# Performance work log

Hardware: AMD Instinct MI355X
Metric: run time of the kernel (lower is better)

## Reference

```python
import jax, jax.numpy as jnp
import numpy as np

B, S, E, H = 2, 2048, 1024, 16
D = E // H  # head_dim = 64


def setup_inputs() -> dict:
    key = jax.random.key(0)
    ks = jax.random.split(key, 12)
    s = 1.0 / np.sqrt(E)
    return {
        "queries": jax.random.normal(ks[0], (B, S, E), jnp.float32),
        "keys": jax.random.normal(ks[1], (B, S, E), jnp.float32),
        "values": jax.random.normal(ks[2], (B, S, E), jnp.float32),
        "mask": jnp.zeros((B, 1, S, S), jnp.float32),
        "Wq": jax.random.normal(ks[3], (E, E), jnp.float32) * s,
        "bq": jnp.zeros((E,), jnp.float32),
        "Wk": jax.random.normal(ks[4], (E, E), jnp.float32) * s,
        "bk": jnp.zeros((E,), jnp.float32),
        "Wv": jax.random.normal(ks[5], (E, E), jnp.float32) * s,
        "bv": jnp.zeros((E,), jnp.float32),
        "Wo": jax.random.normal(ks[6], (E, E), jnp.float32) * s,
        "bo": jnp.zeros((E,), jnp.float32),
    }


def reference(queries, keys, values, mask, Wq, bq, Wk, bk, Wv, bv, Wo, bo):
    # QKV projections, then split heads: [B,S,E] -> [B,H,S,D]
    def split_heads(x):
        return x.reshape(B, S, H, D).transpose(0, 2, 1, 3)

    Q = split_heads(queries @ Wq + bq)
    K = split_heads(keys @ Wk + bk)
    V = split_heads(values @ Wv + bv)
    scale = jnp.sqrt(jnp.asarray(D, jnp.float32))
    # [B,H,S,S] attention scores
    scores = jnp.einsum("bhqd,bhkd->bhqk", Q, K) / scale
    scores = scores + mask * -10000.0
    weights = jax.nn.softmax(scores, axis=-1)
    # [B,H,S,D] -> [B,S,E]
    out = jnp.einsum("bhqk,bhkd->bhqd", weights, V)
    out = out.transpose(0, 2, 1, 3).reshape(B, S, E)
    return out @ Wo + bo
```

## Files before the change

### kernel.cpp

```cpp
#include <hip/hip_runtime.h>
#include <hip/hip_bf16.h>
#include <stdint.h>

#define B_ 2
#define S_ 2048
#define E_ 1024
#define H_ 16
#define D_ 64
#define LOG2E 1.4426950408889634f

typedef unsigned short ubf;
typedef __attribute__((ext_vector_type(8))) short bh8;
typedef __attribute__((ext_vector_type(4))) float fx4;
typedef __attribute__((ext_vector_type(16))) float fx16;

__device__ __forceinline__ ubf f2bf(float f) {
  unsigned u = __float_as_uint(f);
  unsigned r = (u + 0x7fffu + ((u >> 16) & 1u)) >> 16;
  return (ubf)r;
}

__device__ __forceinline__ unsigned cvtpk(float lo, float hi2) {
  unsigned r;
  asm("v_cvt_pk_bf16_f32 %0, %1, %2" : "=v"(r) : "v"(lo), "v"(hi2));
  return r;
}

__device__ __forceinline__ void pl32swap(unsigned& a, unsigned& b) {
  asm("v_permlane32_swap_b32 %0, %1" : "+v"(a), "+v"(b));
}

__device__ __forceinline__ void gl_lds16(const void* g, void* l) {
  __builtin_amdgcn_global_load_lds(
      (const __attribute__((address_space(1))) void*)g,
      (__attribute__((address_space(3))) void*)l, 16, 0, 0);
}

__global__ void prep(const float* __restrict__ q, const float* __restrict__ k,
                     const float* __restrict__ v, const float* __restrict__ mask,
                     ubf* __restrict__ dst0, int* __restrict__ flagarr) {
  const int z = blockIdx.z;
  const int tid = threadIdx.x;
  const int stride = gridDim.x * blockDim.x;
  if (z == 3) {
    int any = 0;
    const int n4m = (B_ * S_ * S_) / 4;
    for (int j = blockIdx.x * blockDim.x + tid; j < n4m; j += stride) {
      float4 x = ((const float4*)mask)[j];
      any |= (x.x != 0.f) | (x.y != 0.f) | (x.z != 0.f) | (x.w != 0.f);
    }
    int wany = __any(any != 0) ? 1 : 0;
    if ((tid & 63) == 0) flagarr[blockIdx.x * 4 + (tid >> 6)] = wany;
    return;
  }
  const float* src = (z == 0) ? q : (z == 1) ? k : v;
  ubf* dst = dst0 + (size_t)z * (B_ * S_ * E_);
  const int n4 = (B_ * S_ * E_) / 4;
  for (int j = blockIdx.x * blockDim.x + tid; j < n4; j += stride) {
    float4 x = ((const float4*)src)[j];
    ushort4 o;
    o.x = f2bf(x.x); o.y = f2bf(x.y); o.z = f2bf(x.z); o.w = f2bf(x.w);
    ((ushort4*)dst)[j] = o;
  }
}

__global__ void wtrans4(const float* __restrict__ Wq, const float* __restrict__ Wk,
                        const float* __restrict__ Wv, const float* __restrict__ Wo,
                        ubf* __restrict__ Wt0) {
  __shared__ float t[32][33];
  int z = blockIdx.z;
  const float* W = (z == 0) ? Wq : (z == 1) ? Wk : (z == 2) ? Wv : Wo;
  ubf* Wt = Wt0 + (size_t)z * (E_ * E_);
  int kb = blockIdx.x, nb = blockIdx.y;
  int c = threadIdx.x & 31, r0 = threadIdx.x >> 5;
#pragma unroll
  for (int rr = 0; rr < 32; rr += 8)
    t[r0 + rr][c] = W[(size_t)(kb * 32 + r0 + rr) * E_ + nb * 32 + c];
  __syncthreads();
#pragma unroll
  for (int rr = 0; rr < 32; rr += 8)
    Wt[(size_t)(nb * 32 + r0 + rr) * E_ + kb * 32 + c] = f2bf(t[c][r0 + rr]);
}

__global__ void __launch_bounds__(256)
gemm_qkv(const ubf* __restrict__ X, const ubf* __restrict__ Wt,
         const float* __restrict__ bq, const float* __restrict__ bk,
         const float* __restrict__ bv, ubf* __restrict__ Out) {
  constexpr int K = 1024;
  __shared__ ubf Asm[2][128 * 32];
  __shared__ ubf Bsm[2][128 * 32];
  const int z = blockIdx.z;
  const ubf* A  = (z == 2) ? (Wt + 2u * 1048576u) : (X + (size_t)z * 4194304u);
  const ubf* Bt = (z == 2) ? (X + 2u * 4194304u) : (Wt + (size_t)z * 1048576u);
  const float* bias = (z == 0) ? bq : (z == 1) ? bk : bv;
  ubf* Cout = Out + (size_t)z * 4194304u;
  const int bm = (z == 2) ? blockIdx.y : blockIdx.x;
  const int bn = (z == 2) ? blockIdx.x : blockIdx.y;

  const int tid = threadIdx.x;
  const int lane = tid & 63, w = tid >> 6;
  const int wm = w >> 1, wn = w & 1;
  const int g = lane >> 4, c15 = lane & 15;

  const fx4 FZ = {0.f, 0.f, 0.f, 0.f};
  fx4 acc[4][4];
#pragma unroll
  for (int m = 0; m < 4; m++)
#pragma unroll
    for (int n = 0; n < 4; n++) acc[m][n] = FZ;

  auto stage = [&](int buf, int k0) {
#pragma unroll
    for (int i = 0; i < 2; i++) {
      int s = i * 256 + tid;
      int row = s >> 2, cc = s & 3;
      int sc = cc ^ (row & 3);
      gl_lds16(A + (size_t)(bm * 128 + row) * K + k0 + sc * 8,
               (char*)&Asm[buf][0] + (i * 256 + (tid & 192)) * 16);
      gl_lds16(Bt + (size_t)(bn * 128 + row) * K + k0 + sc * 8,
               (char*)&Bsm[buf][0] + (i * 256 + (tid & 192)) * 16);
    }
  };

  stage(0, 0);
  __syncthreads();
  for (int t = 0; t < K / 32; t++) {
    int cur = t & 1;
    if (t + 1 < K / 32) stage(cur ^ 1, (t + 1) * 32);
    bh8 a[4], b[4];
#pragma unroll
    for (int m = 0; m < 4; m++) {
      int row = wm * 64 + m * 16 + c15;
      int ch = g ^ (row & 3);
      a[m] = *(const bh8*)((const char*)&Asm[cur][0] + row * 64 + ch * 16);
    }
#pragma unroll
    for (int n = 0; n < 4; n++) {
      int row = wn * 64 + n * 16 + c15;
      int ch = g ^ (row & 3);
      b[n] = *(const bh8*)((const char*)&Bsm[cur][0] + row * 64 + ch * 16);
    }
#pragma unroll
    for (int m = 0; m < 4; m++)
#pragma unroll
      for (int n = 0; n < 4; n++)
        acc[m][n] = __builtin_amdgcn_mfma_f32_16x16x32_bf16(a[m], b[n], acc[m][n], 0, 0, 0);
    __syncthreads();
  }

#pragma unroll
  for (int m = 0; m < 4; m++) {
    int rbase = bm * 128 + wm * 64 + m * 16 + g * 4;
#pragma unroll
    for (int n = 0; n < 4; n++) {
      int col = bn * 128 + wn * 64 + n * 16 + c15;
#pragma unroll
      for (int r = 0; r < 4; r++) {
        int mrow = rbase + r;
        float val = acc[m][n][r];
        if (z <= 1) {
          val = val + bias[col];
          if (z == 0) val *= 0.125f * LOG2E;
          int bb = mrow >> 11, ss = mrow & 2047, hh = col >> 6, dd = col & 63;
          Cout[((size_t)(bb * H_ + hh) * S_ + ss) * D_ + dd] = f2bf(val);
        } else {
          val = val + bias[mrow];
          int bb = col >> 11, ss = col & 2047, hh = mrow >> 6, dd = mrow & 63;
          Cout[((size_t)(bb * H_ + hh) * D_ + dd) * S_ + ss] = f2bf(val);
        }
      }
    }
  }
}

__global__ void __launch_bounds__(256)
gemm_out(const ubf* __restrict__ A, const ubf* __restrict__ Bt,
         const float* __restrict__ bias, float* __restrict__ Cout, int N) {
  constexpr int K = 1024;
  __shared__ ubf Asm[2][128 * 32];
  __shared__ ubf Bsm[2][128 * 32];
  const int tid = threadIdx.x;
  const int lane = tid & 63, w = tid >> 6;
  const int wm = w >> 1, wn = w & 1;
  const int bm = blockIdx.y, bn = blockIdx.x;
  const int g = lane >> 4, c15 = lane & 15;

  const fx4 FZ = {0.f, 0.f, 0.f, 0.f};
  fx4 acc[4][4];
#pragma unroll
  for (int m = 0; m < 4; m++)
#pragma unroll
    for (int n = 0; n < 4; n++) acc[m][n] = FZ;

  auto stage = [&](int buf, int k0) {
#pragma unroll
    for (int i = 0; i < 2; i++) {
      int s = i * 256 + tid;
      int row = s >> 2, cc = s & 3;
      int sc = cc ^ (row & 3);
      gl_lds16(A + (size_t)(bm * 128 + row) * K + k0 + sc * 8,
               (char*)&Asm[buf][0] + (i * 256 + (tid & 192)) * 16);
      gl_lds16(Bt + (size_t)(bn * 128 + row) * K + k0 + sc * 8,
               (char*)&Bsm[buf][0] + (i * 256 + (tid & 192)) * 16);
    }
  };

  stage(0, 0);
  __syncthreads();
  for (int t = 0; t < K / 32; t++) {
    int cur = t & 1;
    if (t + 1 < K / 32) stage(cur ^ 1, (t + 1) * 32);
    bh8 a[4], b[4];
#pragma unroll
    for (int m = 0; m < 4; m++) {
      int row = wm * 64 + m * 16 + c15;
      int ch = g ^ (row & 3);
      a[m] = *(const bh8*)((const char*)&Asm[cur][0] + row * 64 + ch * 16);
    }
#pragma unroll
    for (int n = 0; n < 4; n++) {
      int row = wn * 64 + n * 16 + c15;
      int ch = g ^ (row & 3);
      b[n] = *(const bh8*)((const char*)&Bsm[cur][0] + row * 64 + ch * 16);
    }
#pragma unroll
    for (int m = 0; m < 4; m++)
#pragma unroll
      for (int n = 0; n < 4; n++)
        acc[m][n] = __builtin_amdgcn_mfma_f32_16x16x32_bf16(a[m], b[n], acc[m][n], 0, 0, 0);
    __syncthreads();
  }

#pragma unroll
  for (int m = 0; m < 4; m++) {
    int rbase = bm * 128 + wm * 64 + m * 16 + g * 4;
#pragma unroll
    for (int n = 0; n < 4; n++) {
      int col = bn * 128 + wn * 64 + n * 16 + c15;
#pragma unroll
      for (int r = 0; r < 4; r++)
        Cout[(size_t)(rbase + r) * N + col] = acc[m][n][r] + bias[col];
    }
  }
}

#define ROWQ(r) (((r) & 3) + 8 * ((r) >> 2) + 4 * hi)

#define PV_STEP(KF, W0, W1, W2, W3)                                             \
    {                                                                           \
      unsigned wa[4] = {W0, W1, W2, W3};                                        \
      bh8 pa = *(bh8*)wa;                                                       \
      int ch = (2 * (KF) + hi) ^ (l31 & 7);                                     \
      bh8 bv0 = *(const bh8*)(Vc + l31 * 128 + ch * 16);                        \
      acc0 = __builtin_amdgcn_mfma_f32_32x32x16_bf16(pa, bv0, acc0, 0, 0, 0);   \
      bh8 bv1 = *(const bh8*)(Vc + (32 + l31) * 128 + ch * 16);                 \
      acc1 = __builtin_amdgcn_mfma_f32_32x32x16_bf16(pa, bv1, acc1, 0, 0, 0);   \
    }

__global__ void __launch_bounds__(256, 4)
flash_fast(const ubf* __restrict__ Q, const ubf* __restrict__ Kh,
           const ubf* __restrict__ Vt, float* __restrict__ O0,
           float* __restrict__ O1, float2* __restrict__ ml) {
  __shared__ ubf Ksm[2][64 * 64];
  __shared__ ubf Vsm[2][64 * 64];
  const int tid = threadIdx.x, lane = tid & 63, w = tid >> 6;
  const int l31 = lane & 31, hi = lane >> 5;
  const int bh = blockIdx.x;
  const int qb = blockIdx.y;
  const int half = blockIdx.z;
  const int qg = qb * 128 + w * 32 + l31;
  const int k00 = half * (S_ / 2);
  constexpr int NT = (S_ / 2) / 64;

  const ubf* Qrow = Q + ((size_t)bh * S_ + qg) * D_;
  bh8 q4[4];
#pragma unroll
  for (int kf = 0; kf < 4; kf++) q4[kf] = *(const bh8*)(Qrow + kf * 16 + hi * 8);

  fx16 acc0, acc1, ZF;
#pragma unroll
  for (int i = 0; i < 16; i++) { acc0[i] = 0.f; acc1[i] = 0.f; ZF[i] = 0.f; }
  float2 lr2 = make_float2(0.f, 0.f);

  const ubf* Kg = Kh + (size_t)bh * S_ * D_;
  const ubf* Vg = Vt + (size_t)bh * D_ * S_;

  auto stage = [&](int buf, int k0) {
#pragma unroll
    for (int i = 0; i < 2; i++) {
      int s = i * 256 + tid;
      int row = s >> 3, cc = s & 7;
      int sw = cc ^ (row & 7);
      gl_lds16(Kg + (size_t)(k0 + row) * D_ + sw * 8,
               (char*)&Ksm[buf][0] + (i * 256 + (tid & 192)) * 16);
      gl_lds16(Vg + (size_t)row * S_ + k0 + sw * 8,
               (char*)&Vsm[buf][0] + (i * 256 + (tid & 192)) * 16);
    }
  };

  stage(0, k00);

  for (int t = 0; t < NT; t++) {
    int cur = t & 1;
    if (t + 1 < NT) {
      stage(cur ^ 1, k00 + (t + 1) * 64);
      asm volatile("s_waitcnt vmcnt(4)" ::: "memory");
    } else {
      asm volatile("s_waitcnt vmcnt(0)" ::: "memory");
    }
    __builtin_amdgcn_s_barrier();
    const char* Kc = (const char*)&Ksm[cur][0];
    const char* Vc = (const char*)&Vsm[cur][0];

#pragma unroll
    for (int h2 = 0; h2 < 2; h2++) {
      fx16 sc;
      __builtin_amdgcn_s_setprio(1);
      {
        int ch = hi ^ (l31 & 7);
        bh8 ak = *(const bh8*)(Kc + (h2 * 32 + l31) * 128 + ch * 16);
        sc = __builtin_amdgcn_mfma_f32_32x32x16_bf16(ak, q4[0], ZF, 0, 0, 0);
      }
#pragma unroll
      for (int kf = 1; kf < 4; kf++) {
        int ch = (2 * kf + hi) ^ (l31 & 7);
        bh8 ak = *(const bh8*)(Kc + (h2 * 32 + l31) * 128 + ch * 16);
        sc = __builtin_amdgcn_mfma_f32_32x32x16_bf16(ak, q4[kf], sc, 0, 0, 0);
      }
      __builtin_amdgcn_s_setprio(0);

#pragma unroll
      for (int i = 0; i < 8; i++) {
        float p0 = exp2f(sc[2 * i]);
        float p1 = exp2f(sc[2 * i + 1]);
        sc[2 * i] = p0; sc[2 * i + 1] = p1;
        lr2.x += p0; lr2.y += p1;
      }

      unsigned pk[8];
#pragma unroll
      for (int i = 0; i < 8; i++) pk[i] = cvtpk(sc[2 * i], sc[2 * i + 1]);
      pl32swap(pk[0], pk[2]); pl32swap(pk[1], pk[3]);
      pl32swap(pk[4], pk[6]); pl32swap(pk[5], pk[7]);

      __builtin_amdgcn_s_setprio(1);
      PV_STEP(2 * h2,     pk[0], pk[1], pk[2], pk[3])
      PV_STEP(2 * h2 + 1, pk[4], pk[5], pk[6], pk[7])
      __builtin_amdgcn_s_setprio(0);
    }
    __builtin_amdgcn_s_barrier();
  }

  float lrun = lr2.x + lr2.y;
  float lsum = lrun + __shfl_xor(lrun, 32);
  float* Obase = half ? O1 : O0;
#pragma unroll
  for (int r = 0; r < 16; r++) {
    int q2 = ROWQ(r);
    size_t rowbase = ((size_t)bh * S_ + qb * 128 + w * 32 + q2) * D_;
    Obase[rowbase + l31] = acc0[r];
    Obase[rowbase + 32 + l31] = acc1[r];
  }
  if (hi == 0) {
    int sq = qb * 128 + w * 32 + l31;
    ml[(size_t)half * (32 * S_) + bh * S_ + sq] = make_float2(0.0f, lsum);
  }
}

__global__ void __launch_bounds__(256)
combine(const float* __restrict__ O0, const float* __restrict__ O1,
        const float2* __restrict__ ml, ubf* __restrict__ AO) {
  int tid = blockIdx.x * 256 + threadIdx.x;
  int row = tid >> 4, dq = tid & 15;
  int bh = row >> 11, s = row & 2047;
  float2 m0 = ml[row];
  float2 m1 = ml[32 * S_ + row];
  float m = fmaxf(m0.x, m1.x);
  float w0 = exp2f(m0.x - m), w1 = exp2f(m1.x - m);
  float inv = 1.0f / (m0.y * w0 + m1.y * w1);
  float4 a = *(const float4*)(O0 + (size_t)row * D_ + dq * 4);
  float4 c = *(const float4*)(O1 + (size_t)row * D_ + dq * 4);
  ushort4 o;
  o.x = f2bf((a.x * w0 + c.x * w1) * inv);
  o.y = f2bf((a.y * w0 + c.y * w1) * inv);
  o.z = f2bf((a.z * w0 + c.z * w1) * inv);
  o.w = f2bf((a.w * w0 + c.w * w1) * inv);
  int b_ = bh >> 4, h = bh & 15;
  *(ushort4*)(AO + ((size_t)(b_ * S_ + s)) * E_ + h * 64 + dq * 4) = o;
}

__global__ void __launch_bounds__(256, 4)
flash_masked(const ubf* __restrict__ Q, const ubf* __restrict__ Kh,
             const ubf* __restrict__ Vt, const float* __restrict__ mask,
             const int* __restrict__ flagarr, ubf* __restrict__ AO) {
  __shared__ int anyf;
  if (threadIdx.x == 0) anyf = 0;
  __syncthreads();
  {
    int a = 0;
#pragma unroll
    for (int i = 0; i < 8; i++) a |= flagarr[threadIdx.x + i * 256];
    if (a) anyf = 1;
  }
  __syncthreads();
  if (anyf == 0) return;

  __shared__ ubf Ksm[2][64 * 64];
  __shared__ ubf Vsm[2][64 * 64];
  const int tid = threadIdx.x, lane = tid & 63, w = tid >> 6;
  const int l31 = lane & 31, hi = lane >> 5;
  const int bh = blockIdx.x;
  const int qb = blockIdx.y;
  const int b = bh >> 4, h = bh & 15;
  const int qg = qb * 128 + w * 32 + l31;
  constexpr int NT = S_ / 64;

  const ubf* Qrow = Q + ((size_t)bh * S_ + qg) * D_;
  bh8 q4[4];
#pragma unroll
  for (int kf = 0; kf < 4; kf++) q4[kf] = *(const bh8*)(Qrow + kf * 16 + hi * 8);

  fx16 acc0, acc1;
#pragma unroll
  for (int i = 0; i < 16; i++) { acc0[i] = 0.f; acc1[i] = 0.f; }
  float mrun = -3.0e38f, lrun = 0.f;

  const ubf* Kg = Kh + (size_t)bh * S_ * D_;
  const ubf* Vg = Vt + (size_t)bh * D_ * S_;

  auto stage = [&](int buf, int k0) {
#pragma unroll
    for (int i = 0; i < 2; i++) {
      int s = i * 256 + tid;
      int row = s >> 3, cc = s & 7;
      int sw = cc ^ (row & 7);
      gl_lds16(Kg + (size_t)(k0 + row) * D_ + sw * 8,
               (char*)&Ksm[buf][0] + (i * 256 + (tid & 192)) * 16);
      gl_lds16(Vg + (size_t)row * S_ + k0 + sw * 8,
               (char*)&Vsm[buf][0] + (i * 256 + (tid & 192)) * 16);
    }
  };

  stage(0, 0);
  __syncthreads();

  for (int t = 0; t < NT; t++) {
    int cur = t & 1;
    if (t + 1 < NT) stage(cur ^ 1, (t + 1) * 64);
    const char* Kc = (const char*)&Ksm[cur][0];
    const char* Vc = (const char*)&Vsm[cur][0];

#pragma unroll
    for (int h2 = 0; h2 < 2; h2++) {
      fx16 sc;
#pragma unroll
      for (int i = 0; i < 16; i++) sc[i] = 0.f;
#pragma unroll
      for (int kf = 0; kf < 4; kf++) {
        int ch = (2 * kf + hi) ^ (l31 & 7);
        bh8 ak = *(const bh8*)(Kc + (h2 * 32 + l31) * 128 + ch * 16);
        sc = __builtin_amdgcn_mfma_f32_32x32x16_bf16(ak, q4[kf], sc, 0, 0, 0);
      }
      const float* mq = mask + ((size_t)(b * S_ + qg)) * S_ + t * 64 + h2 * 32;
#pragma unroll
      for (int r = 0; r < 16; r++)
        sc[r] += mq[ROWQ(r)] * (-14426.950408889634f);

      float pm = sc[0];
#pragma unroll
      for (int r = 1; r < 16; r++) pm = fmaxf(pm, sc[r]);
      pm = fmaxf(pm, __shfl_xor(pm, 32));
      if (__any(pm - mrun > 11.5415603f)) {
        float mnew = fmaxf(mrun, pm);
        float al = exp2f(mrun - mnew);
        lrun *= al;
#pragma unroll
        for (int r = 0; r < 16; r++) {
          float alr = __shfl(al, ROWQ(r));
          acc0[r] *= alr;
          acc1[r] *= alr;
        }
        mrun = mnew;
      }
      float rsv[4] = {0.f, 0.f, 0.f, 0.f};
#pragma unroll
      for (int i = 0; i < 16; i++) {
        float p = exp2f(sc[i] - mrun);
        sc[i] = p;
        rsv[i & 3] += p;
      }
      lrun += (rsv[0] + rsv[1]) + (rsv[2] + rsv[3]);

      unsigned pk[8];
#pragma unroll
      for (int i = 0; i < 8; i++) pk[i] = cvtpk(sc[2 * i], sc[2 * i + 1]);
      pl32swap(pk[0], pk[2]); pl32swap(pk[1], pk[3]);
      pl32swap(pk[4], pk[6]); pl32swap(pk[5], pk[7]);

      PV_STEP(2 * h2,     pk[0], pk[1], pk[2], pk[3])
      PV_STEP(2 * h2 + 1, pk[4], pk[5], pk[6], pk[7])
    }
    __syncthreads();
  }

  float ltot = lrun + __shfl_xor(lrun, 32);
#pragma unroll
  for (int r = 0; r < 16; r++) {
    int q2 = ROWQ(r);
    float linv = 1.0f / __shfl(ltot, q2);
    size_t base = ((size_t)(b * S_ + qb * 128 + w * 32 + q2)) * E_ + h * 64;
    AO[base + l31] = f2bf(acc0[r] * linv);
    AO[base + 32 + l31] = f2bf(acc1[r] * linv);
  }
}

extern "C" void kernel_launch(void* const* d_in, const int* in_sizes, int n_in,
                              void* d_out, int out_size, void* d_ws, size_t ws_size,
                              hipStream_t stream) {
  (void)in_sizes; (void)n_in; (void)out_size; (void)ws_size;
  const float* q  = (const float*)d_in[0];
  const float* k  = (const float*)d_in[1];
  const float* v  = (const float*)d_in[2];
  const float* mask = (const float*)d_in[3];
  const float* Wq = (const float*)d_in[4];
  const float* bq = (const float*)d_in[5];
  const float* Wk = (const float*)d_in[6];
  const float* bk = (const float*)d_in[7];
  const float* Wv = (const float*)d_in[8];
  const float* bv = (const float*)d_in[9];
  const float* Wo = (const float*)d_in[10];
  const float* bo = (const float*)d_in[11];

  char* ws = (char*)d_ws;
  ubf* X    = (ubf*)(ws);
  ubf* Wt0  = (ubf*)(ws + 25165824);
  ubf* Qh   = (ubf*)(ws + 33554432);
  ubf* Kh   = (ubf*)(ws + 41943040);
  ubf* Vt   = (ubf*)(ws + 50331648);
  ubf* AO   = (ubf*)(ws + 58720256);
  int* flagarr = (int*)(ws + 67108864);
  float*  O0p = (float*)(ws);
  float2* mlp = (float2*)(ws + 16777216);
  float*  O1p = (float*)d_out;

  ubf* Wot = Wt0 + 3145728;

  prep<<<dim3(512, 1, 4), 256, 0, stream>>>(q, k, v, mask, X, flagarr);
  wtrans4<<<dim3(32, 32, 4), 256, 0, stream>>>(Wq, Wk, Wv, Wo, Wt0);

  gemm_qkv<<<dim3(32, 8, 3), 256, 0, stream>>>(X, Wt0, bq, bk, bv, Qh);

  flash_fast<<<dim3(32, 16, 2), 256, 0, stream>>>(Qh, Kh, Vt, O0p, O1p, mlp);
  combine<<<4096, 256, 0, stream>>>(O0p, O1p, mlp, AO);
  flash_masked<<<dim3(32, 16), 256, 0, stream>>>(Qh, Kh, Vt, mask, flagarr, AO);

  gemm_out<<<dim3(8, 32), 256, 0, stream>>>(AO, Wot, bo, (float*)d_out, 1024);
}
```

Measured before the change: 164.6 us.

## Double per-wave query rows in flash kernel and pipeline GEMM LDS staging

In flash_fast each wave now handles 64 query rows as two 32-row tiles that share every K and V fragment read from LDS. The block shrinks to 128 threads, so each thread issues four async loads per buffer, with the wait count adjusted to match. This halves LDS reads per MFMA but doubles the accumulator registers and halves the waves per block. The two GEMM kernels change their LDS swizzle to XOR on (row>>1)&3, replace __syncthreads with explicit vmcnt waits and raw barriers for prefetch overlap, and raise wave priority around the MFMA block.

```diff
diff --git a/kernel.cpp b/kernel.cpp
--- a/kernel.cpp
+++ b/kernel.cpp
@@ -114,7 +114,7 @@
     for (int i = 0; i < 2; i++) {
       int s = i * 256 + tid;
       int row = s >> 2, cc = s & 3;
-      int sc = cc ^ (row & 3);
+      int sc = cc ^ ((row >> 1) & 3);
       gl_lds16(A + (size_t)(bm * 128 + row) * K + k0 + sc * 8,
                (char*)&Asm[buf][0] + (i * 256 + (tid & 192)) * 16);
       gl_lds16(Bt + (size_t)(bn * 128 + row) * K + k0 + sc * 8,
@@ -123,29 +123,36 @@
   };
 
   stage(0, 0);
-  __syncthreads();
   for (int t = 0; t < K / 32; t++) {
     int cur = t & 1;
-    if (t + 1 < K / 32) stage(cur ^ 1, (t + 1) * 32);
+    if (t + 1 < K / 32) {
+      stage(cur ^ 1, (t + 1) * 32);
+      asm volatile("s_waitcnt vmcnt(4)" ::: "memory");
+    } else {
+      asm volatile("s_waitcnt vmcnt(0)" ::: "memory");
+    }
+    __builtin_amdgcn_s_barrier();
     bh8 a[4], b[4];
 #pragma unroll
     for (int m = 0; m < 4; m++) {
       int row = wm * 64 + m * 16 + c15;
-      int ch = g ^ (row & 3);
+      int ch = g ^ ((row >> 1) & 3);
       a[m] = *(const bh8*)((const char*)&Asm[cur][0] + row * 64 + ch * 16);
     }
 #pragma unroll
     for (int n = 0; n < 4; n++) {
       int row = wn * 64 + n * 16 + c15;
-      int ch = g ^ (row & 3);
+      int ch = g ^ ((row >> 1) & 3);
       b[n] = *(const bh8*)((const char*)&Bsm[cur][0] + row * 64 + ch * 16);
     }
+    __builtin_amdgcn_s_setprio(1);
 #pragma unroll
     for (int m = 0; m < 4; m++)
 #pragma unroll
       for (int n = 0; n < 4; n++)
         acc[m][n] = __builtin_amdgcn_mfma_f32_16x16x32_bf16(a[m], b[n], acc[m][n], 0, 0, 0);
-    __syncthreads();
+    __builtin_amdgcn_s_setprio(0);
+    __builtin_amdgcn_s_barrier();
   }
 
 #pragma unroll
@@ -197,7 +204,7 @@
     for (int i = 0; i < 2; i++) {
       int s = i * 256 + tid;
       int row = s >> 2, cc = s & 3;
-      int sc = cc ^ (row & 3);
+      int sc = cc ^ ((row >> 1) & 3);
       gl_lds16(A + (size_t)(bm * 128 + row) * K + k0 + sc * 8,
                (char*)&Asm[buf][0] + (i * 256 + (tid & 192)) * 16);
       gl_lds16(Bt + (size_t)(bn * 128 + row) * K + k0 + sc * 8,
@@ -206,29 +213,36 @@
   };
 
   stage(0, 0);
-  __syncthreads();
   for (int t = 0; t < K / 32; t++) {
     int cur = t & 1;
-    if (t + 1 < K / 32) stage(cur ^ 1, (t + 1) * 32);
+    if (t + 1 < K / 32) {
+      stage(cur ^ 1, (t + 1) * 32);
+      asm volatile("s_waitcnt vmcnt(4)" ::: "memory");
+    } else {
+      asm volatile("s_waitcnt vmcnt(0)" ::: "memory");
+    }
+    __builtin_amdgcn_s_barrier();
     bh8 a[4], b[4];
 #pragma unroll
     for (int m = 0; m < 4; m++) {
       int row = wm * 64 + m * 16 + c15;
-      int ch = g ^ (row & 3);
+      int ch = g ^ ((row >> 1) & 3);
       a[m] = *(const bh8*)((const char*)&Asm[cur][0] + row * 64 + ch * 16);
     }
 #pragma unroll
     for (int n = 0; n < 4; n++) {
       int row = wn * 64 + n * 16 + c15;
-      int ch = g ^ (row & 3);
+      int ch = g ^ ((row >> 1) & 3);
       b[n] = *(const bh8*)((const char*)&Bsm[cur][0] + row * 64 + ch * 16);
     }
+    __builtin_amdgcn_s_setprio(1);
 #pragma unroll
     for (int m = 0; m < 4; m++)
 #pragma unroll
       for (int n = 0; n < 4; n++)
         acc[m][n] = __builtin_amdgcn_mfma_f32_16x16x32_bf16(a[m], b[n], acc[m][n], 0, 0, 0);
-    __syncthreads();
+    __builtin_amdgcn_s_setprio(0);
+    __builtin_amdgcn_s_barrier();
   }
 
 #pragma unroll
@@ -246,18 +260,7 @@
 
 #define ROWQ(r) (((r) & 3) + 8 * ((r) >> 2) + 4 * hi)
 
-#define PV_STEP(KF, W0, W1, W2, W3)                                             \
-    {                                                                           \
-      unsigned wa[4] = {W0, W1, W2, W3};                                        \
-      bh8 pa = *(bh8*)wa;                                                       \
-      int ch = (2 * (KF) + hi) ^ (l31 & 7);                                     \
-      bh8 bv0 = *(const bh8*)(Vc + l31 * 128 + ch * 16);                        \
-      acc0 = __builtin_amdgcn_mfma_f32_32x32x16_bf16(pa, bv0, acc0, 0, 0, 0);   \
-      bh8 bv1 = *(const bh8*)(Vc + (32 + l31) * 128 + ch * 16);                 \
-      acc1 = __builtin_amdgcn_mfma_f32_32x32x16_bf16(pa, bv1, acc1, 0, 0, 0);   \
-    }
-
-__global__ void __launch_bounds__(256, 4)
+__global__ void __launch_bounds__(128, 2)
 flash_fast(const ubf* __restrict__ Q, const ubf* __restrict__ Kh,
            const ubf* __restrict__ Vt, float* __restrict__ O0,
            float* __restrict__ O1, float2* __restrict__ ml) {
@@ -268,33 +271,38 @@
   const int bh = blockIdx.x;
   const int qb = blockIdx.y;
   const int half = blockIdx.z;
-  const int qg = qb * 128 + w * 32 + l31;
   const int k00 = half * (S_ / 2);
   constexpr int NT = (S_ / 2) / 64;
-
-  const ubf* Qrow = Q + ((size_t)bh * S_ + qg) * D_;
-  bh8 q4[4];
-#pragma unroll
-  for (int kf = 0; kf < 4; kf++) q4[kf] = *(const bh8*)(Qrow + kf * 16 + hi * 8);
-
-  fx16 acc0, acc1, ZF;
-#pragma unroll
-  for (int i = 0; i < 16; i++) { acc0[i] = 0.f; acc1[i] = 0.f; ZF[i] = 0.f; }
-  float2 lr2 = make_float2(0.f, 0.f);
+  const int qbase = qb * 128 + w * 64;
+
+  const ubf* QrowA = Q + ((size_t)bh * S_ + qbase + l31) * D_;
+  bh8 q4a[4], q4b[4];
+#pragma unroll
+  for (int kf = 0; kf < 4; kf++) {
+    q4a[kf] = *(const bh8*)(QrowA + kf * 16 + hi * 8);
+    q4b[kf] = *(const bh8*)(QrowA + 32 * D_ + kf * 16 + hi * 8);
+  }
+
+  fx16 acc0a, acc1a, acc0b, acc1b, ZF;
+#pragma unroll
+  for (int i = 0; i < 16; i++) {
+    acc0a[i] = 0.f; acc1a[i] = 0.f; acc0b[i] = 0.f; acc1b[i] = 0.f; ZF[i] = 0.f;
+  }
+  float lra = 0.f, lrb = 0.f;
 
   const ubf* Kg = Kh + (size_t)bh * S_ * D_;
   const ubf* Vg = Vt + (size_t)bh * D_ * S_;
 
   auto stage = [&](int buf, int k0) {
 #pragma unroll
-    for (int i = 0; i < 2; i++) {
-      int s = i * 256 + tid;
+    for (int i = 0; i < 4; i++) {
+      int s = i * 128 + tid;
       int row = s >> 3, cc = s & 7;
       int sw = cc ^ (row & 7);
       gl_lds16(Kg + (size_t)(k0 + row) * D_ + sw * 8,
-               (char*)&Ksm[buf][0] + (i * 256 + (tid & 192)) * 16);
+               (char*)&Ksm[buf][0] + (i * 128 + (tid & 64)) * 16);
       gl_lds16(Vg + (size_t)row * S_ + k0 + sw * 8,
-               (char*)&Vsm[buf][0] + (i * 256 + (tid & 192)) * 16);
+               (char*)&Vsm[buf][0] + (i * 128 + (tid & 64)) * 16);
     }
   };
 
@@ -304,7 +312,7 @@
     int cur = t & 1;
     if (t + 1 < NT) {
       stage(cur ^ 1, k00 + (t + 1) * 64);
-      asm volatile("s_waitcnt vmcnt(4)" ::: "memory");
+      asm volatile("s_waitcnt vmcnt(8)" ::: "memory");
     } else {
       asm volatile("s_waitcnt vmcnt(0)" ::: "memory");
     }
@@ -314,56 +322,80 @@
 
 #pragma unroll
     for (int h2 = 0; h2 < 2; h2++) {
-      fx16 sc;
+      fx16 sa, sb;
       __builtin_amdgcn_s_setprio(1);
-      {
-        int ch = hi ^ (l31 & 7);
-        bh8 ak = *(const bh8*)(Kc + (h2 * 32 + l31) * 128 + ch * 16);
-        sc = __builtin_amdgcn_mfma_f32_32x32x16_bf16(ak, q4[0], ZF, 0, 0, 0);
-      }
-#pragma unroll
-      for (int kf = 1; kf < 4; kf++) {
+#pragma unroll
+      for (int kf = 0; kf < 4; kf++) {
         int ch = (2 * kf + hi) ^ (l31 & 7);
         bh8 ak = *(const bh8*)(Kc + (h2 * 32 + l31) * 128 + ch * 16);
-        sc = __builtin_amdgcn_mfma_f32_32x32x16_bf16(ak, q4[kf], sc, 0, 0, 0);
+        sa = __builtin_amdgcn_mfma_f32_32x32x16_bf16(ak, q4a[kf], kf ? sa : ZF, 0, 0, 0);
+        sb = __builtin_amdgcn_mfma_f32_32x32x16_bf16(ak, q4b[kf], kf ? sb : ZF, 0, 0, 0);
       }
       __builtin_amdgcn_s_setprio(0);
 
+      float ra0 = 0.f, ra1 = 0.f, rb0 = 0.f, rb1 = 0.f;
 #pragma unroll
       for (int i = 0; i < 8; i++) {
-        float p0 = exp2f(sc[2 * i]);
-        float p1 = exp2f(sc[2 * i + 1]);
-        sc[2 * i] = p0; sc[2 * i + 1] = p1;
-        lr2.x += p0; lr2.y += p1;
-      }
-
-      unsigned pk[8];
-#pragma unroll
-      for (int i = 0; i < 8; i++) pk[i] = cvtpk(sc[2 * i], sc[2 * i + 1]);
-      pl32swap(pk[0], pk[2]); pl32swap(pk[1], pk[3]);
-      pl32swap(pk[4], pk[6]); pl32swap(pk[5], pk[7]);
+        float a0 = exp2f(sa[2 * i]);
+        float a1 = exp2f(sa[2 * i + 1]);
+        float b0 = exp2f(sb[2 * i]);
+        float b1 = exp2f(sb[2 * i + 1]);
+        sa[2 * i] = a0; sa[2 * i + 1] = a1;
+        sb[2 * i] = b0; sb[2 * i + 1] = b1;
+        ra0 += a0; ra1 += a1; rb0 += b0; rb1 += b1;
+      }
+      lra += ra0 + ra1;
+      lrb += rb0 + rb1;
+
+      unsigned pka[8], pkb[8];
+#pragma unroll
+      for (int i = 0; i < 8; i++) {
+        pka[i] = cvtpk(sa[2 * i], sa[2 * i + 1]);
+        pkb[i] = cvtpk(sb[2 * i], sb[2 * i + 1]);
+      }
+      pl32swap(pka[0], pka[2]); pl32swap(pka[1], pka[3]);
+      pl32swap(pka[4], pka[6]); pl32swap(pka[5], pka[7]);
+      pl32swap(pkb[0], pkb[2]); pl32swap(pkb[1], pkb[3]);
+      pl32swap(pkb[4], pkb[6]); pl32swap(pkb[5], pkb[7]);
 
       __builtin_amdgcn_s_setprio(1);
-      PV_STEP(2 * h2,     pk[0], pk[1], pk[2], pk[3])
-      PV_STEP(2 * h2 + 1, pk[4], pk[5], pk[6], pk[7])
+#pragma unroll
+      for (int kk = 0; kk < 2; kk++) {
+        int KF = 2 * h2 + kk;
+        int ch = (2 * KF + hi) ^ (l31 & 7);
+        bh8 bv0 = *(const bh8*)(Vc + l31 * 128 + ch * 16);
+        bh8 bv1 = *(const bh8*)(Vc + (32 + l31) * 128 + ch * 16);
+        unsigned waA[4] = {pka[4 * kk], pka[4 * kk + 1], pka[4 * kk + 2], pka[4 * kk + 3]};
+        unsigned waB[4] = {pkb[4 * kk], pkb[4 * kk + 1], pkb[4 * kk + 2], pkb[4 * kk + 3]};
+        bh8 pa = *(bh8*)waA;
+        bh8 pb = *(bh8*)waB;
+        acc0a = __builtin_amdgcn_mfma_f32_32x32x16_bf16(pa, bv0, acc0a, 0, 0, 0);
+        acc1a = __builtin_amdgcn_mfma_f32_32x32x16_bf16(pa, bv1, acc1a, 0, 0, 0);
+        acc0b = __builtin_amdgcn_mfma_f32_32x32x16_bf16(pb, bv0, acc0b, 0, 0, 0);
+        acc1b = __builtin_amdgcn_mfma_f32_32x32x16_bf16(pb, bv1, acc1b, 0, 0, 0);
+      }
       __builtin_amdgcn_s_setprio(0);
     }
     __builtin_amdgcn_s_barrier();
   }
 
-  float lrun = lr2.x + lr2.y;
-  float lsum = lrun + __shfl_xor(lrun, 32);
+  float lsa = lra + __shfl_xor(lra, 32);
+  float lsb = lrb + __shfl_xor(lrb, 32);
   float* Obase = half ? O1 : O0;
 #pragma unroll
   for (int r = 0; r < 16; r++) {
     int q2 = ROWQ(r);
-    size_t rowbase = ((size_t)bh * S_ + qb * 128 + w * 32 + q2) * D_;
-    Obase[rowbase + l31] = acc0[r];
-    Obase[rowbase + 32 + l31] = acc1[r];
+    size_t rowA = ((size_t)bh * S_ + qbase + q2) * D_;
+    Obase[rowA + l31] = acc0a[r];
+    Obase[rowA + 32 + l31] = acc1a[r];
+    size_t rowB = rowA + (size_t)32 * D_;
+    Obase[rowB + l31] = acc0b[r];
+    Obase[rowB + 32 + l31] = acc1b[r];
   }
   if (hi == 0) {
-    int sq = qb * 128 + w * 32 + l31;
-    ml[(size_t)half * (32 * S_) + bh * S_ + sq] = make_float2(0.0f, lsum);
+    size_t mbase = (size_t)half * (32 * S_) + bh * S_;
+    ml[mbase + qbase + l31] = make_float2(0.0f, lsa);
+    ml[mbase + qbase + 32 + l31] = make_float2(0.0f, lsb);
   }
 }
 
@@ -389,6 +421,17 @@
   *(ushort4*)(AO + ((size_t)(b_ * S_ + s)) * E_ + h * 64 + dq * 4) = o;
 }
 
+#define PV_STEP(KF, W0, W1, W2, W3)                                             \
+    {                                                                           \
+      unsigned wa[4] = {W0, W1, W2, W3};                                        \
+      bh8 pa = *(bh8*)wa;                                                       \
+      int ch = (2 * (KF) + hi) ^ (l31 & 7);                                     \
+      bh8 bv0 = *(const bh8*)(Vc + l31 * 128 + ch * 16);                        \
+      acc0 = __builtin_amdgcn_mfma_f32_32x32x16_bf16(pa, bv0, acc0, 0, 0, 0);   \
+      bh8 bv1 = *(const bh8*)(Vc + (32 + l31) * 128 + ch * 16);                 \
+      acc1 = __builtin_amdgcn_mfma_f32_32x32x16_bf16(pa, bv1, acc1, 0, 0, 0);   \
+    }
+
 __global__ void __launch_bounds__(256, 4)
 flash_masked(const ubf* __restrict__ Q, const ubf* __restrict__ Kh,
              const ubf* __restrict__ Vt, const float* __restrict__ mask,
@@ -550,7 +593,7 @@
 
   gemm_qkv<<<dim3(32, 8, 3), 256, 0, stream>>>(X, Wt0, bq, bk, bv, Qh);
 
-  flash_fast<<<dim3(32, 16, 2), 256, 0, stream>>>(Qh, Kh, Vt, O0p, O1p, mlp);
+  flash_fast<<<dim3(32, 16, 2), 128, 0, stream>>>(Qh, Kh, Vt, O0p, O1p, mlp);
   combine<<<4096, 256, 0, stream>>>(O0p, O1p, mlp, AO);
   flash_masked<<<dim3(32, 16), 256, 0, stream>>>(Qh, Kh, Vt, mask, flagarr, AO);
 
```

Measured after the change: 163.9 us. About the same (-0.4%).

## Shrink GEMM tiles for more blocks and use vmcnt-based pipelined waits

Applied to the files above, without the earlier changes.

The QKV projection GEMM drops from 128x128 to 128x64 tiles and the output GEMM from 128x128 to 64x64 tiles. This raises block counts (1536 and 1024) so more of the GPU's compute units are busy and occupancy goes up. Each K-step now waits with explicit s_waitcnt vmcnt on the async global-to-LDS loads plus a raw barrier instead of __syncthreads. MFMA issue is wrapped in setprio, and the LDS swizzle changes to XOR on (row>>1)&3. Smaller tiles mean less operand reuse per block and more global traffic. The flash PV macro is rewritten as a loop that loads both V fragments before the MFMAs.

```diff
diff --git a/kernel.cpp b/kernel.cpp
--- a/kernel.cpp
+++ b/kernel.cpp
@@ -82,20 +82,21 @@
     Wt[(size_t)(nb * 32 + r0 + rr) * E_ + kb * 32 + c] = f2bf(t[c][r0 + rr]);
 }
 
-__global__ void __launch_bounds__(256)
+__global__ void __launch_bounds__(256, 6)
 gemm_qkv(const ubf* __restrict__ X, const ubf* __restrict__ Wt,
          const float* __restrict__ bq, const float* __restrict__ bk,
          const float* __restrict__ bv, ubf* __restrict__ Out) {
   constexpr int K = 1024;
   __shared__ ubf Asm[2][128 * 32];
-  __shared__ ubf Bsm[2][128 * 32];
+  __shared__ ubf Bsm[2][64 * 32];
   const int z = blockIdx.z;
   const ubf* A  = (z == 2) ? (Wt + 2u * 1048576u) : (X + (size_t)z * 4194304u);
   const ubf* Bt = (z == 2) ? (X + 2u * 4194304u) : (Wt + (size_t)z * 1048576u);
   const float* bias = (z == 0) ? bq : (z == 1) ? bk : bv;
   ubf* Cout = Out + (size_t)z * 4194304u;
-  const int bm = (z == 2) ? blockIdx.y : blockIdx.x;
-  const int bn = (z == 2) ? blockIdx.x : blockIdx.y;
+  const int bx = blockIdx.x;
+  const int bm = (z == 2) ? (bx >> 6) : (bx >> 4);
+  const int bn = (z == 2) ? (bx & 63) : (bx & 15);
 
   const int tid = threadIdx.x;
   const int lane = tid & 63, w = tid >> 6;
@@ -103,57 +104,68 @@
   const int g = lane >> 4, c15 = lane & 15;
 
   const fx4 FZ = {0.f, 0.f, 0.f, 0.f};
-  fx4 acc[4][4];
+  fx4 acc[4][2];
 #pragma unroll
   for (int m = 0; m < 4; m++)
 #pragma unroll
-    for (int n = 0; n < 4; n++) acc[m][n] = FZ;
+    for (int n = 0; n < 2; n++) acc[m][n] = FZ;
 
   auto stage = [&](int buf, int k0) {
 #pragma unroll
     for (int i = 0; i < 2; i++) {
       int s = i * 256 + tid;
       int row = s >> 2, cc = s & 3;
-      int sc = cc ^ (row & 3);
+      int sc = cc ^ ((row >> 1) & 3);
       gl_lds16(A + (size_t)(bm * 128 + row) * K + k0 + sc * 8,
                (char*)&Asm[buf][0] + (i * 256 + (tid & 192)) * 16);
-      gl_lds16(Bt + (size_t)(bn * 128 + row) * K + k0 + sc * 8,
-               (char*)&Bsm[buf][0] + (i * 256 + (tid & 192)) * 16);
+    }
+    {
+      int row = tid >> 2, cc = tid & 3;
+      int sc = cc ^ ((row >> 1) & 3);
+      gl_lds16(Bt + (size_t)(bn * 64 + row) * K + k0 + sc * 8,
+               (char*)&Bsm[buf][0] + (tid & 192) * 16);
     }
   };
 
   stage(0, 0);
-  __syncthreads();
   for (int t = 0; t < K / 32; t++) {
     int cur = t & 1;
-    if (t + 1 < K / 32) stage(cur ^ 1, (t + 1) * 32);
-    bh8 a[4], b[4];
+    if (t + 1 < K / 32) {
+      stage(cur ^ 1, (t + 1) * 32);
+      asm volatile("s_waitcnt vmcnt(3)" ::: "memory");
+    } else {
+      asm volatile("s_waitcnt vmcnt(0)" ::: "memory");
+    }
+    __builtin_amdgcn_s_barrier();
+    bh8 a[4], b[2];
 #pragma unroll
     for (int m = 0; m < 4; m++) {
       int row = wm * 64 + m * 16 + c15;
-      int ch = g ^ (row & 3);
+      int ch = g ^ ((row >> 1) & 3);
       a[m] = *(const bh8*)((const char*)&Asm[cur][0] + row * 64 + ch * 16);
     }
 #pragma unroll
-    for (int n = 0; n < 4; n++) {
-      int row = wn * 64 + n * 16 + c15;
-      int ch = g ^ (row & 3);
+    for (int n = 0; n < 2; n++) {
+      int row = wn * 32 + n * 16 + c15;
+      int ch = g ^ ((row >> 1) & 3);
       b[n] = *(const bh8*)((const char*)&Bsm[cur][0] + row * 64 + ch * 16);
     }
+    __builtin_amdgcn_s_setprio(1);
 #pragma unroll
     for (int m = 0; m < 4; m++)
 #pragma unroll
-      for (int n = 0; n < 4; n++)
+      for (int n = 0; n < 2; n++)
         acc[m][n] = __builtin_amdgcn_mfma_f32_16x16x32_bf16(a[m], b[n], acc[m][n], 0, 0, 0);
-    __syncthreads();
+    __builtin_amdgcn_s_setprio(0);
+    __builtin_amdgcn_s_barrier();
   }
 
 #pragma unroll
   for (int m = 0; m < 4; m++) {
     int rbase = bm * 128 + wm * 64 + m * 16 + g * 4;
 #pragma unroll
-    for (int n = 0; n < 4; n++) {
-      int col = bn * 128 + wn * 64 + n * 16 + c15;
+    for (int n = 0; n < 2; n++) {
+      int col = bn * 64 + wn * 32 + n * 16 + c15;
 #pragma unroll
       for (int r = 0; r < 4; r++) {
         int mrow = rbase + r;
@@ -173,12 +185,12 @@
   }
 }
 
-__global__ void __launch_bounds__(256)
+__global__ void __launch_bounds__(256, 4)
 gemm_out(const ubf* __restrict__ A, const ubf* __restrict__ Bt,
          const float* __restrict__ bias, float* __restrict__ Cout, int N) {
   constexpr int K = 1024;
-  __shared__ ubf Asm[2][128 * 32];
-  __shared__ ubf Bsm[2][128 * 32];
+  __shared__ ubf Asm[2][64 * 32];
+  __shared__ ubf Bsm[2][64 * 32];
   const int tid = threadIdx.x;
   const int lane = tid & 63, w = tid >> 6;
   const int wm = w >> 1, wn = w & 1;
@@ -186,57 +198,60 @@
   const int g = lane >> 4, c15 = lane & 15;
 
   const fx4 FZ = {0.f, 0.f, 0.f, 0.f};
-  fx4 acc[4][4];
-#pragma unroll
-  for (int m = 0; m < 4; m++)
-#pragma unroll
-    for (int n = 0; n < 4; n++) acc[m][n] = FZ;
+  fx4 acc[2][2];
+#pragma unroll
+  for (int m = 0; m < 2; m++)
+#pragma unroll
+    for (int n = 0; n < 2; n++) acc[m][n] = FZ;
 
   auto stage = [&](int buf, int k0) {
-#pragma unroll
-    for (int i = 0; i < 2; i++) {
-      int s = i * 256 + tid;
-      int row = s >> 2, cc = s & 3;
-      int sc = cc ^ (row & 3);
-      gl_lds16(A + (size_t)(bm * 128 + row) * K + k0 + sc * 8,
-               (char*)&Asm[buf][0] + (i * 256 + (tid & 192)) * 16);
-      gl_lds16(Bt + (size_t)(bn * 128 + row) * K + k0 + sc * 8,
-               (char*)&Bsm[buf][0] + (i * 256 + (tid & 192)) * 16);
-    }
+    int row = tid >> 2, cc = tid & 3;
+    int sc = cc ^ ((row >> 1) & 3);
+    gl_lds16(A + (size_t)(bm * 64 + row) * K + k0 + sc * 8,
+             (char*)&Asm[buf][0] + (tid & 192) * 16);
+    gl_lds16(Bt + (size_t)(bn * 64 + row) * K + k0 + sc * 8,
+             (char*)&Bsm[buf][0] + (tid & 192) * 16);
   };
 
   stage(0, 0);
-  __syncthreads();
   for (int t = 0; t < K / 32; t++) {
     int cur = t & 1;
-    if (t + 1 < K / 32) stage(cur ^ 1, (t + 1) * 32);
-    bh8 a[4], b[4];
-#pragma unroll
-    for (int m = 0; m < 4; m++) {
-      int row = wm * 64 + m * 16 + c15;
-      int ch = g ^ (row & 3);
+    if (t + 1 < K / 32) {
+      stage(cur ^ 1, (t + 1) * 32);
+      asm volatile("s_waitcnt vmcnt(2)" ::: "memory");
+    } else {
+      asm volatile("s_waitcnt vmcnt(0)" ::: "memory");
+    }
+    __builtin_amdgcn_s_barrier();
+    bh8 a[2], b[2];
+#pragma unroll
+    for (int m = 0; m < 2; m++) {
+      int row = wm * 32 + m * 16 + c15;
+      int ch = g ^ ((row >> 1) & 3);
       a[m] = *(const bh8*)((const char*)&Asm[cur][0] + row * 64 + ch * 16);
     }
 #pragma unroll
-    for (int n = 0; n < 4; n++) {
-      int row = wn * 64 + n * 16 + c15;
-      int ch = g ^ (row & 3);
+    for (int n = 0; n < 2; n++) {
+      int row = wn * 32 + n * 16 + c15;
+      int ch = g ^ ((row >> 1) & 3);
       b[n] = *(const bh8*)((const char*)&Bsm[cur][0] + row * 64 + ch * 16);
     }
-#pragma unroll
-    for (int m = 0; m < 4; m++)
-#pragma unroll
-      for (int n = 0; n < 4; n++)
+    __builtin_amdgcn_s_setprio(1);
+#pragma unroll
+    for (int m = 0; m < 2; m++)
+#pragma unroll
+      for (int n = 0; n < 2; n++)
         acc[m][n] = __builtin_amdgcn_mfma_f32_16x16x32_bf16(a[m], b[n], acc[m][n], 0, 0, 0);
-    __syncthreads();
-  }
-
-#pragma unroll
-  for (int m = 0; m < 4; m++) {
-    int rbase = bm * 128 + wm * 64 + m * 16 + g * 4;
-#pragma unroll
-    for (int n = 0; n < 4; n++) {
-      int col = bn * 128 + wn * 64 + n * 16 + c15;
+    __builtin_amdgcn_s_setprio(0);
+    __builtin_amdgcn_s_barrier();
+  }
+
+#pragma unroll
+  for (int m = 0; m < 2; m++) {
+    int rbase = bm * 64 + wm * 32 + m * 16 + g * 4;
+#pragma unroll
+    for (int n = 0; n < 2; n++) {
+      int col = bn * 64 + wn * 32 + n * 16 + c15;
 #pragma unroll
       for (int r = 0; r < 4; r++)
         Cout[(size_t)(rbase + r) * N + col] = acc[m][n][r] + bias[col];
@@ -245,17 +260,6 @@
 }
 
 #define ROWQ(r) (((r) & 3) + 8 * ((r) >> 2) + 4 * hi)
-
-#define PV_STEP(KF, W0, W1, W2, W3)                                             \
-    {                                                                           \
-      unsigned wa[4] = {W0, W1, W2, W3};                                        \
-      bh8 pa = *(bh8*)wa;                                                       \
-      int ch = (2 * (KF) + hi) ^ (l31 & 7);                                     \
-      bh8 bv0 = *(const bh8*)(Vc + l31 * 128 + ch * 16);                        \
-      acc0 = __builtin_amdgcn_mfma_f32_32x32x16_bf16(pa, bv0, acc0, 0, 0, 0);   \
-      bh8 bv1 = *(const bh8*)(Vc + (32 + l31) * 128 + ch * 16);                 \
-      acc1 = __builtin_amdgcn_mfma_f32_32x32x16_bf16(pa, bv1, acc1, 0, 0, 0);   \
-    }
 
 __global__ void __launch_bounds__(256, 4)
 flash_fast(const ubf* __restrict__ Q, const ubf* __restrict__ Kh,
@@ -344,8 +348,17 @@
       pl32swap(pk[4], pk[6]); pl32swap(pk[5], pk[7]);
 
       __builtin_amdgcn_s_setprio(1);
-      PV_STEP(2 * h2,     pk[0], pk[1], pk[2], pk[3])
-      PV_STEP(2 * h2 + 1, pk[4], pk[5], pk[6], pk[7])
+#pragma unroll
+      for (int kk = 0; kk < 2; kk++) {
+        int KF = 2 * h2 + kk;
+        int ch = (2 * KF + hi) ^ (l31 & 7);
+        bh8 bv0 = *(const bh8*)(Vc + l31 * 128 + ch * 16);
+        bh8 bv1 = *(const bh8*)(Vc + (32 + l31) * 128 + ch * 16);
+        unsigned wa[4] = {pk[4 * kk], pk[4 * kk + 1], pk[4 * kk + 2], pk[4 * kk + 3]};
+        bh8 pa = *(bh8*)wa;
+        acc0 = __builtin_amdgcn_mfma_f32_32x32x16_bf16(pa, bv0, acc0, 0, 0, 0);
+        acc1 = __builtin_amdgcn_mfma_f32_32x32x16_bf16(pa, bv1, acc1, 0, 0, 0);
+      }
       __builtin_amdgcn_s_setprio(0);
     }
     __builtin_amdgcn_s_barrier();
@@ -389,6 +402,17 @@
   *(ushort4*)(AO + ((size_t)(b_ * S_ + s)) * E_ + h * 64 + dq * 4) = o;
 }
 
+#define PV_STEP(KF, W0, W1, W2, W3)                                             \
+    {                                                                           \
+      unsigned wa[4] = {W0, W1, W2, W3};                                        \
+      bh8 pa = *(bh8*)wa;                                                       \
+      int ch = (2 * (KF) + hi) ^ (l31 & 7);                                     \
+      bh8 bv0 = *(const bh8*)(Vc + l31 * 128 + ch * 16);                        \
+      acc0 = __builtin_amdgcn_mfma_f32_32x32x16_bf16(pa, bv0, acc0, 0, 0, 0);   \
+      bh8 bv1 = *(const bh8*)(Vc + (32 + l31) * 128 + ch * 16);                 \
+      acc1 = __builtin_amdgcn_mfma_f32_32x32x16_bf16(pa, bv1, acc1, 0, 0, 0);   \
+    }
+
 __global__ void __launch_bounds__(256, 4)
 flash_masked(const ubf* __restrict__ Q, const ubf* __restrict__ Kh,
              const ubf* __restrict__ Vt, const float* __restrict__ mask,
@@ -548,11 +572,11 @@
   prep<<<dim3(512, 1, 4), 256, 0, stream>>>(q, k, v, mask, X, flagarr);
   wtrans4<<<dim3(32, 32, 4), 256, 0, stream>>>(Wq, Wk, Wv, Wo, Wt0);
 
-  gemm_qkv<<<dim3(32, 8, 3), 256, 0, stream>>>(X, Wt0, bq, bk, bv, Qh);
+  gemm_qkv<<<dim3(512, 1, 3), 256, 0, stream>>>(X, Wt0, bq, bk, bv, Qh);
 
   flash_fast<<<dim3(32, 16, 2), 256, 0, stream>>>(Qh, Kh, Vt, O0p, O1p, mlp);
   combine<<<4096, 256, 0, stream>>>(O0p, O1p, mlp, AO);
   flash_masked<<<dim3(32, 16), 256, 0, stream>>>(Qh, Kh, Vt, mask, flagarr, AO);
 
-  gemm_out<<<dim3(8, 32), 256, 0, stream>>>(AO, Wot, bo, (float*)d_out, 1024);
-}
+  gemm_out<<<dim3(16, 64), 256, 0, stream>>>(AO, Wot, bo, (float*)d_out, 1024);
+}
```

Result: faster. 159.3 us (-3.2%).
